# Performance work log

Measured on AMD Instinct MI355X. Metric: run time of the kernel, lower is better.

## Reference

```python
import jax, jax.numpy as jnp
import numpy as np

N_MICS = 8
REF_MIC = 0
DIAG_LOAD = 1e-5
PI_ITERS = 30  # power-iteration steps for principal eigenvector of Phi_nn^-1 Phi_ss


def setup_inputs() -> dict:
    key = jax.random.key(0)
    k1, k2, k3, k4 = jax.random.split(key, 4)
    B, M, F, T = 8, N_MICS, 257, 2000
    return {
        "spec_re": jax.random.normal(k1, (B, M, F, T), dtype=jnp.float32),
        "spec_im": jax.random.normal(k2, (B, M, F, T), dtype=jnp.float32),
        "speech_mask": jax.random.uniform(k3, (B, F, T), dtype=jnp.float32),
        "noise_mask": jax.random.uniform(k4, (B, F, T), dtype=jnp.float32),
    }


def _mvdr(spec_re, spec_im, speech_mask, noise_mask):
    # (B, M, F, T) complex STFT -> (B, F, M, T) for per-(batch, freq) processing
    Y = (spec_re + 1j * spec_im).astype(jnp.complex64)
    Y = jnp.transpose(Y, (0, 2, 1, 3))  # (B, F, M, T)
    M = Y.shape[2]

    def masked_cov(mask):  # mask: (B, F, T) real
        msum = mask.sum(-1) + 1e-8                       # (B, F)
        Yw = Y * mask[:, :, None, :]                      # (B, F, M, T)
        Phi = jnp.einsum('bfmt,bfnt->bfmn', Yw, Y.conj())  # (B, F, M, M)
        return Phi / msum[..., None, None]

    Phi_ss = masked_cov(speech_mask)
    eye = jnp.eye(M, dtype=jnp.complex64)
    Phi_nn = masked_cov(noise_mask) + DIAG_LOAD * eye

    Phi_nn_inv = jnp.linalg.inv(Phi_nn)                   # batched (B, F, M, M)
    G = jnp.einsum('bfmn,bfnk->bfmk', Phi_nn_inv, Phi_ss)

    # Principal eigenvector of G via power iteration (G has real, nonnegative
    # eigenvalues since it is similar to a Hermitian-PSD generalized pencil),
    # matching torch.linalg.eig + argmax(eigenvalues.real) up to scale.
    v = jnp.ones(G.shape[:-1], dtype=jnp.complex64)       # (B, F, M)
    for _ in range(PI_ITERS):
        v = jnp.einsum('bfmn,bfn->bfm', G, v)
        v = v / (jnp.linalg.norm(v, axis=-1, keepdims=True) + 1e-12)

    # Relative transfer function normalized to reference mic (removes scale)
    rtf = v / (v[..., REF_MIC:REF_MIC + 1] + 1e-8)        # (B, F, M)

    d = jnp.einsum('bfmn,bfn->bfm', Phi_nn_inv, rtf)      # Phi_nn^-1 rtf
    denom = jnp.einsum('bfm,bfm->bf', rtf.conj(), d).real + 1e-8
    w = d / denom[..., None]                              # (B, F, M) MVDR weights

    enhanced = jnp.einsum('bfm,bfmt->bft', w.conj(), Y)   # (B, F, T) complex
    return enhanced


def reference(spec_re, spec_im, speech_mask, noise_mask):
    return _mvdr(spec_re, spec_im, speech_mask, noise_mask)
```

## Files before the change

kernel.cpp:

```cpp
#include <hip/hip_runtime.h>

#define B_DIM 8
#define M_MICS 8
#define F_DIM 257
#define T_DIM 2000
#define NPROB (B_DIM * F_DIM)
#define TILE 256
#define NFULL 7
#define TAILW 208

__device__ float g_w[NPROB * 16];

#define GLOAD_LDS(g, s) __builtin_amdgcn_global_load_lds(                       \
    (const __attribute__((address_space(1))) void*)(g),                         \
    (__attribute__((address_space(3))) void*)(s), 16, 0, 0)


#define PAIR_ACC(a, bb, k)                                              \
    {                                                                   \
        const float pr = yr[a][u] * yr[bb][u] + yi[a][u] * yi[bb][u];   \
        const float pi = yi[a][u] * yr[bb][u] - yr[a][u] * yi[bb][u];   \
        acc[(k) + 0] += msv[u] * pr;                                    \
        acc[(k) + 1] += msv[u] * pi;                                    \
        acc[(k) + 2] += mnv[u] * pr;                                    \
        acc[(k) + 3] += mnv[u] * pi;                                    \
    }

#define LOADM(k, mic)                                                             \
    {                                                                             \
        const float4 vr_ = *reinterpret_cast<const float4*>(&lds[bb][mic][4 * l]);      \
        const float4 vi_ = *reinterpret_cast<const float4*>(&lds[bb][8 + (mic)][4 * l]);\
        yr[k][0] = vr_.x; yr[k][1] = vr_.y; yr[k][2] = vr_.z; yr[k][3] = vr_.w;   \
        yi[k][0] = vi_.x; yi[k][1] = vi_.y; yi[k][2] = vi_.z; yi[k][3] = vi_.w;   \
    }

#define PAIR_BODY(LOADS, ACCS, KM)                                      \
    {                                                                   \
        float yr[KM][4], yi[KM][4];                                     \
        LOADS                                                           \
        _Pragma("unroll")                                               \
        for (int u = 0; u < 4; ++u) { ACCS }                            \
    }

__launch_bounds__(512, 4)
__global__ void cov_solve_kernel(const float* __restrict__ sre, const float* __restrict__ sim,
                                 const float* __restrict__ smask, const float* __restrict__ nmask)
{
    const int f = blockIdx.x, b = blockIdx.y, tid = threadIdx.x;
    const int h = tid >> 6, l = tid & 63;

    __shared__ float lds[2][18][TILE];
    __shared__ float sG[8][20];

    const size_t mrow = (size_t)F_DIM * T_DIM;
    const size_t base_bf = ((size_t)(b * M_MICS) * F_DIM + f) * T_DIM;
    const size_t mbase   = ((size_t)b * F_DIM + f) * T_DIM;

    const float* g_re = sre + base_bf + (size_t)h * mrow;
    const float* g_im = sim + base_bf + (size_t)h * mrow;
    const float* g_ms = smask + mbase;
    const float* g_mn = nmask + mbase;

    float acc[18];
#pragma unroll
    for (int i = 0; i < 18; ++i) acc[i] = 0.f;

    auto STAGE = [&](int bb, int toff, int tw) {
        if (4 * l < tw) {
            GLOAD_LDS(g_re + toff + 4 * l, &lds[bb][h][0]);
            GLOAD_LDS(g_im + toff + 4 * l, &lds[bb][8 + h][0]);
            if (h == 0)      GLOAD_LDS(g_ms + toff + 4 * l, &lds[bb][16][0]);
            else if (h == 1) GLOAD_LDS(g_mn + toff + 4 * l, &lds[bb][17][0]);
        }
    };

    auto COMPUTE = [&](int bb) {
        float msv[4], mnv[4];
        {
            const float4 v = *reinterpret_cast<const float4*>(&lds[bb][16][4 * l]);
            msv[0] = v.x; msv[1] = v.y; msv[2] = v.z; msv[3] = v.w;
        }
        {
            const float4 v = *reinterpret_cast<const float4*>(&lds[bb][17][4 * l]);
            mnv[0] = v.x; mnv[1] = v.y; mnv[2] = v.z; mnv[3] = v.w;
        }
        if (h == 0) {
            acc[0] += msv[0] + msv[1] + msv[2] + msv[3];
            acc[1] += mnv[0] + mnv[1] + mnv[2] + mnv[3];
#pragma unroll
            for (int m = 0; m < 8; ++m) {
                const float4 re4 = *reinterpret_cast<const float4*>(&lds[bb][m][4 * l]);
                const float4 im4 = *reinterpret_cast<const float4*>(&lds[bb][8 + m][4 * l]);
                const float rr[4] = { re4.x, re4.y, re4.z, re4.w };
                const float ii[4] = { im4.x, im4.y, im4.z, im4.w };
#pragma unroll
                for (int u = 0; u < 4; ++u) {
                    const float pd = rr[u] * rr[u] + ii[u] * ii[u];
                    acc[2 + m]  += msv[u] * pd;
                    acc[10 + m] += mnv[u] * pd;
                }
            }
        } else if (h == 1) {
            PAIR_BODY(LOADM(0,0) LOADM(1,1) LOADM(2,2) LOADM(3,3) LOADM(4,4),
                      PAIR_ACC(0,1,0) PAIR_ACC(0,2,4) PAIR_ACC(0,3,8) PAIR_ACC(0,4,12), 5)
        } else if (h == 2) {
            PAIR_BODY(LOADM(0,0) LOADM(1,1) LOADM(2,2) LOADM(3,5) LOADM(4,6) LOADM(5,7),
                      PAIR_ACC(0,3,0) PAIR_ACC(0,4,4) PAIR_ACC(0,5,8) PAIR_ACC(1,2,12), 6)
        } else if (h == 3) {
            PAIR_BODY(LOADM(0,1) LOADM(1,3) LOADM(2,4) LOADM(3,5) LOADM(4,6),
                      PAIR_ACC(0,1,0) PAIR_ACC(0,2,4) PAIR_ACC(0,3,8) PAIR_ACC(0,4,12), 5)
        } else if (h == 4) {
            PAIR_BODY(LOADM(0,1) LOADM(1,2) LOADM(2,3) LOADM(3,4) LOADM(4,5) LOADM(5,7),
                      PAIR_ACC(0,5,0) PAIR_ACC(1,2,4) PAIR_ACC(1,3,8) PAIR_ACC(1,4,12), 6)
        } else if (h == 5) {
            PAIR_BODY(LOADM(0,2) LOADM(1,3) LOADM(2,4) LOADM(3,5) LOADM(4,6) LOADM(5,7),
                      PAIR_ACC(0,4,0) PAIR_ACC(0,5,4) PAIR_ACC(1,2,8) PAIR_ACC(1,3,12), 6)
        } else if (h == 6) {
            PAIR_BODY(LOADM(0,3) LOADM(1,4) LOADM(2,5) LOADM(3,6) LOADM(4,7),
                      PAIR_ACC(0,3,0) PAIR_ACC(0,4,4) PAIR_ACC(1,2,8) PAIR_ACC(1,3,12), 5)
        } else {
            PAIR_BODY(LOADM(0,4) LOADM(1,5) LOADM(2,6) LOADM(3,7),
                      PAIR_ACC(0,3,0) PAIR_ACC(1,2,4) PAIR_ACC(1,3,8) PAIR_ACC(2,3,12), 4)
        }
    };

    STAGE(0, 0, TILE);
    __syncthreads();
#pragma unroll 1
    for (int t = 0; t < NFULL; ++t) {
        if (t < NFULL - 1) STAGE((t + 1) & 1, (t + 1) * TILE, TILE);
        else               STAGE(1, NFULL * TILE, TAILW);
        const int bb = t & 1;
        COMPUTE(bb);
        __syncthreads();
    }
    if (4 * l < TAILW) {
        const int bb = 1;
        COMPUTE(bb);
    }

#pragma unroll
    for (int i = 0; i < 18; ++i) {
        acc[i] += __shfl_xor(acc[i], 1, 64);
        acc[i] += __shfl_xor(acc[i], 2, 64);
        acc[i] += __shfl_xor(acc[i], 4, 64);
        acc[i] += __shfl_xor(acc[i], 8, 64);
        acc[i] += __shfl_xor(acc[i], 16, 64);
        acc[i] += __shfl_xor(acc[i], 32, 64);
    }
    if (l == 0) {
#pragma unroll
        for (int i = 0; i < 18; ++i) sG[h][i] = acc[i];
    }
    __syncthreads();

    if (tid < 64) {
        const int r = tid >> 3, cc = tid & 7;
        const float Ssum = sG[0][0] + 1e-8f;
        const float Nsum = sG[0][1] + 1e-8f;

        float ssr, ssi, ar, ai;
        if (r == cc) {
            ssr = sG[0][2 + r] / Ssum;  ssi = 0.f;
            ar  = sG[0][10 + r] / Nsum + 1e-5f;  ai = 0.f;
        } else {
            const int mm  = (r < cc) ? r : cc;
            const int nn2 = (r < cc) ? cc : r;
            const int q = mm * 8 - mm * (mm + 1) / 2 + nn2 - mm - 1;
            const int g = 1 + (q >> 2);
            const int basei = 4 * (q & 3);
            const float sgn = (r < cc) ? 1.f : -1.f;
            ssr = sG[g][basei] / Ssum;
            ssi = sgn * sG[g][basei + 1] / Ssum;
            ar  = sG[g][basei + 2] / Nsum;
            ai  = sgn * sG[g][basei + 3] / Nsum;
        }

        float br = (r == cc) ? 1.f : 0.f, bi = 0.f;
        for (int k = 0; k < 8; ++k) {
            const float pr = __shfl(ar, k * 9, 64);
            const float pi = __shfl(ai, k * 9, 64);
            const float den = pr * pr + pi * pi;
            const float qr = pr / den, qi = -pi / den;
            const bool isk = (r == k);
            const float ar2 = ar * qr - ai * qi;
            const float ai2 = ar * qi + ai * qr;
            const float br2 = br * qr - bi * qi;
            const float bi2 = br * qi + bi * qr;
            ar = isk ? ar2 : ar; ai = isk ? ai2 : ai;
            br = isk ? br2 : br; bi = isk ? bi2 : bi;
            const float rar = __shfl(ar, k * 8 + cc, 64);
            const float rai = __shfl(ai, k * 8 + cc, 64);
            const float rbr = __shfl(br, k * 8 + cc, 64);
            const float rbi = __shfl(bi, k * 8 + cc, 64);
            const float fr = __shfl(ar, r * 8 + k, 64);
            const float fi = __shfl(ai, r * 8 + k, 64);
            const float uar = ar - (fr * rar - fi * rai);
            const float uai = ai - (fr * rai + fi * rar);
            const float ubr = br - (fr * rbr - fi * rbi);
            const float ubi = bi - (fr * rbi + fi * rbr);
            ar = isk ? ar : uar; ai = isk ? ai : uai;
            br = isk ? br : ubr; bi = isk ? bi : ubi;
        }

        float gr = 0.f, gi = 0.f;
        for (int k = 0; k < 8; ++k) {
            const float ir = __shfl(br, r * 8 + k, 64);
            const float ii = __shfl(bi, r * 8 + k, 64);
            const float skr = __shfl(ssr, k * 8 + cc, 64);
            const float ski = __shfl(ssi, k * 8 + cc, 64);
            gr += ir * skr - ii * ski;
            gi += ir * ski + ii * skr;
        }

        float vr = 1.f, vi = 0.f;
        for (int itp = 0; itp < 30; ++itp) {
            float wr2 = gr * vr - gi * vi;
            float wi2 = gr * vi + gi * vr;
            wr2 += __shfl_xor(wr2, 1, 64); wi2 += __shfl_xor(wi2, 1, 64);
            wr2 += __shfl_xor(wr2, 2, 64); wi2 += __shfl_xor(wi2, 2, 64);
            wr2 += __shfl_xor(wr2, 4, 64); wi2 += __shfl_xor(wi2, 4, 64);
            float nrm = wr2 * wr2 + wi2 * wi2;
            nrm += __shfl_xor(nrm, 8, 64);
            nrm += __shfl_xor(nrm, 16, 64);
            nrm += __shfl_xor(nrm, 32, 64);
            const float inv = 1.f / (sqrtf(nrm) + 1e-12f);
            wr2 *= inv; wi2 *= inv;
            vr = __shfl(wr2, cc * 9, 64);
            vi = __shfl(wi2, cc * 9, 64);
        }

        const float v0r = __shfl(vr, 0, 64) + 1e-8f;
        const float v0i = __shfl(vi, 0, 64);
        const float dd = v0r * v0r + v0i * v0i;
        const float rtr = (vr * v0r + vi * v0i) / dd;
        const float rti = (vi * v0r - vr * v0i) / dd;

        float dr = br * rtr - bi * rti;
        float di = br * rti + bi * rtr;
        dr += __shfl_xor(dr, 1, 64); di += __shfl_xor(di, 1, 64);
        dr += __shfl_xor(dr, 2, 64); di += __shfl_xor(di, 2, 64);
        dr += __shfl_xor(dr, 4, 64); di += __shfl_xor(di, 4, 64);

        float qden = (r == cc) ? (rtr * dr + rti * di) : 0.f;
        qden += __shfl_xor(qden, 1, 64); qden += __shfl_xor(qden, 2, 64);
        qden += __shfl_xor(qden, 4, 64); qden += __shfl_xor(qden, 8, 64);
        qden += __shfl_xor(qden, 16, 64); qden += __shfl_xor(qden, 32, 64);
        qden += 1e-8f;

        if (cc == 0) {
            const int p = b * F_DIM + f;
            g_w[p * 16 + r]     = dr / qden;
            g_w[p * 16 + 8 + r] = di / qden;
        }
    }
}

__launch_bounds__(256, 8)
__global__ void apply_kernel(const float* __restrict__ sre, const float* __restrict__ sim,
                             float* __restrict__ out, int out_mode)
{
    const int f = blockIdx.x, b = blockIdx.y, z = blockIdx.z;
    const int tid = threadIdx.x;
    __shared__ float sW[16];
    const int p = b * F_DIM + f;
    if (tid < 16) sW[tid] = g_w[p * 16 + tid];
    __syncthreads();

    const int t0 = z * 512 + 2 * tid;
    if (t0 >= T_DIM) return;

    const size_t mrow = (size_t)F_DIM * T_DIM;
    const size_t base_bf = ((size_t)(b * M_MICS) * F_DIM + f) * T_DIM;
    const size_t mbase   = ((size_t)b * F_DIM + f) * T_DIM;

    float er0 = 0.f, ei0 = 0.f, er1 = 0.f, ei1 = 0.f;
#pragma unroll
    for (int m = 0; m < 8; ++m) {
        const float2 vr2 = *reinterpret_cast<const float2*>(sre + base_bf + (size_t)m * mrow + t0);
        const float2 vi2 = *reinterpret_cast<const float2*>(sim + base_bf + (size_t)m * mrow + t0);
        const float wr = sW[m], wi = sW[8 + m];
        er0 += wr * vr2.x + wi * vi2.x;
        ei0 += wr * vi2.x - wi * vr2.x;
        er1 += wr * vr2.y + wi * vi2.y;
        ei1 += wr * vi2.y - wi * vr2.y;
    }
    if (out_mode == 2) {
        *reinterpret_cast<float4*>(out + 2 * (mbase + t0)) = make_float4(er0, ei0, er1, ei1);
    } else {
        *reinterpret_cast<float2*>(out + mbase + t0) = make_float2(er0, er1);
    }
}

extern "C" void kernel_launch(void* const* d_in, const int* in_sizes, int n_in,
                              void* d_out, int out_size, void* d_ws, size_t ws_size,
                              hipStream_t stream)
{
    const float* sre   = (const float*)d_in[0];
    const float* sim   = (const float*)d_in[1];
    const float* smask = (const float*)d_in[2];
    const float* nmask = (const float*)d_in[3];
    float* out = (float*)d_out;

    const int mode = (out_size >= 2 * B_DIM * F_DIM * T_DIM) ? 2 : 1;

    cov_solve_kernel<<<dim3(F_DIM, B_DIM), 512, 0, stream>>>(sre, sim, smask, nmask);
    apply_kernel<<<dim3(F_DIM, B_DIM, 4), 256, 0, stream>>>(sre, sim, out, mode);
}
```

Baseline: 178.4 us.

## Split covariance over time chunks, rebalance wave work, separate batched solve kernel

The covariance kernel now splits the 2000-frame time axis into two chunks via a third grid dimension. It writes partial covariance sums to a global scratch buffer. A new solve kernel adds the two partials and runs the inversion, power iteration and MVDR weight computation, packing four problems per block with one wavefront each. The pair assignment across the eight wavefronts is rebalanced so each does a similar number of mic-pair products. This is meant to raise parallelism, even out per-wave work and stop 448 threads sitting idle during the serial solve tail. The cost is an extra kernel launch and a global round-trip for the partial covariances.

```diff
diff --git a/kernel.cpp b/kernel.cpp
--- a/kernel.cpp
+++ b/kernel.cpp
@@ -6,9 +6,11 @@
 #define T_DIM 2000
 #define NPROB (B_DIM * F_DIM)
 #define TILE 256
-#define NFULL 7
-#define TAILW 208
-
+#define CHUNK 1000
+#define NTILE 4
+#define TAILW 232
+
+__device__ float g_cov[NPROB * 2 * 144];
 __device__ float g_w[NPROB * 16];
 
 #define GLOAD_LDS(g, s) __builtin_amdgcn_global_load_lds(                       \
@@ -16,54 +18,55 @@
     (__attribute__((address_space(3))) void*)(s), 16, 0, 0)
 
 
-#define PAIR_ACC(a, bb, k)                                              \
+#define PAIR_ACC(a, bb2, k)                                             \
     {                                                                   \
-        const float pr = yr[a][u] * yr[bb][u] + yi[a][u] * yi[bb][u];   \
-        const float pi = yi[a][u] * yr[bb][u] - yr[a][u] * yi[bb][u];   \
+        const float pr = yr[a][u] * yr[bb2][u] + yi[a][u] * yi[bb2][u]; \
+        const float pi = yi[a][u] * yr[bb2][u] - yr[a][u] * yi[bb2][u]; \
         acc[(k) + 0] += msv[u] * pr;                                    \
         acc[(k) + 1] += msv[u] * pi;                                    \
         acc[(k) + 2] += mnv[u] * pr;                                    \
         acc[(k) + 3] += mnv[u] * pi;                                    \
     }
 
-#define LOADM(k, mic)                                                             \
-    {                                                                             \
+#define LOADM(k, mic)                                                                   \
+    {                                                                                   \
         const float4 vr_ = *reinterpret_cast<const float4*>(&lds[bb][mic][4 * l]);      \
         const float4 vi_ = *reinterpret_cast<const float4*>(&lds[bb][8 + (mic)][4 * l]);\
-        yr[k][0] = vr_.x; yr[k][1] = vr_.y; yr[k][2] = vr_.z; yr[k][3] = vr_.w;   \
-        yi[k][0] = vi_.x; yi[k][1] = vi_.y; yi[k][2] = vi_.z; yi[k][3] = vi_.w;   \
-    }
-
-#define PAIR_BODY(LOADS, ACCS, KM)                                      \
-    {                                                                   \
-        float yr[KM][4], yi[KM][4];                                     \
-        LOADS                                                           \
-        _Pragma("unroll")                                               \
-        for (int u = 0; u < 4; ++u) { ACCS }                            \
+        yr[k][0] = vr_.x; yr[k][1] = vr_.y; yr[k][2] = vr_.z; yr[k][3] = vr_.w;         \
+        yi[k][0] = vi_.x; yi[k][1] = vi_.y; yi[k][2] = vi_.z; yi[k][3] = vi_.w;         \
+    }
+
+#define MASKS4                                                                   \
+    float msv[4], mnv[4];                                                        \
+    {                                                                            \
+        const float4 v = *reinterpret_cast<const float4*>(&lds[bb][16][4 * l]);  \
+        msv[0] = v.x; msv[1] = v.y; msv[2] = v.z; msv[3] = v.w;                  \
+        const float4 w = *reinterpret_cast<const float4*>(&lds[bb][17][4 * l]);  \
+        mnv[0] = w.x; mnv[1] = w.y; mnv[2] = w.z; mnv[3] = w.w;                  \
     }
 
 __launch_bounds__(512, 4)
-__global__ void cov_solve_kernel(const float* __restrict__ sre, const float* __restrict__ sim,
-                                 const float* __restrict__ smask, const float* __restrict__ nmask)
+__global__ void cov_kernel(const float* __restrict__ sre, const float* __restrict__ sim,
+                           const float* __restrict__ smask, const float* __restrict__ nmask)
 {
-    const int f = blockIdx.x, b = blockIdx.y, tid = threadIdx.x;
+    const int f = blockIdx.x, b = blockIdx.y, c = blockIdx.z;
+    const int tid = threadIdx.x;
     const int h = tid >> 6, l = tid & 63;
 
     __shared__ float lds[2][18][TILE];
-    __shared__ float sG[8][20];
 
     const size_t mrow = (size_t)F_DIM * T_DIM;
-    const size_t base_bf = ((size_t)(b * M_MICS) * F_DIM + f) * T_DIM;
-    const size_t mbase   = ((size_t)b * F_DIM + f) * T_DIM;
+    const size_t base_bf = ((size_t)(b * M_MICS) * F_DIM + f) * T_DIM + (size_t)c * CHUNK;
+    const size_t mbase   = ((size_t)b * F_DIM + f) * T_DIM + (size_t)c * CHUNK;
 
     const float* g_re = sre + base_bf + (size_t)h * mrow;
     const float* g_im = sim + base_bf + (size_t)h * mrow;
     const float* g_ms = smask + mbase;
     const float* g_mn = nmask + mbase;
 
-    float acc[18];
-#pragma unroll
-    for (int i = 0; i < 18; ++i) acc[i] = 0.f;
+    float acc[24];
+#pragma unroll
+    for (int i = 0; i < 24; ++i) acc[i] = 0.f;
 
     auto STAGE = [&](int bb, int toff, int tw) {
         if (4 * l < tw) {
@@ -74,73 +77,98 @@
         }
     };
 
-    auto COMPUTE = [&](int bb) {
-        float msv[4], mnv[4];
-        {
-            const float4 v = *reinterpret_cast<const float4*>(&lds[bb][16][4 * l]);
-            msv[0] = v.x; msv[1] = v.y; msv[2] = v.z; msv[3] = v.w;
-        }
-        {
-            const float4 v = *reinterpret_cast<const float4*>(&lds[bb][17][4 * l]);
-            mnv[0] = v.x; mnv[1] = v.y; mnv[2] = v.z; mnv[3] = v.w;
-        }
+    auto COMPUTE = [&](int bb, int tw) {
+        if (4 * l >= tw) return;
+        MASKS4
         if (h == 0) {
             acc[0] += msv[0] + msv[1] + msv[2] + msv[3];
             acc[1] += mnv[0] + mnv[1] + mnv[2] + mnv[3];
 #pragma unroll
-            for (int m = 0; m < 8; ++m) {
-                const float4 re4 = *reinterpret_cast<const float4*>(&lds[bb][m][4 * l]);
-                const float4 im4 = *reinterpret_cast<const float4*>(&lds[bb][8 + m][4 * l]);
+            for (int j = 0; j < 4; ++j) {
+                const float4 re4 = *reinterpret_cast<const float4*>(&lds[bb][j][4 * l]);
+                const float4 im4 = *reinterpret_cast<const float4*>(&lds[bb][8 + j][4 * l]);
                 const float rr[4] = { re4.x, re4.y, re4.z, re4.w };
                 const float ii[4] = { im4.x, im4.y, im4.z, im4.w };
 #pragma unroll
                 for (int u = 0; u < 4; ++u) {
                     const float pd = rr[u] * rr[u] + ii[u] * ii[u];
-                    acc[2 + m]  += msv[u] * pd;
-                    acc[10 + m] += mnv[u] * pd;
+                    acc[2 + j] += msv[u] * pd;
+                    acc[6 + j] += mnv[u] * pd;
                 }
             }
+        } else if (h == 7) {
+#pragma unroll
+            for (int j = 0; j < 4; ++j) {
+                const float4 re4 = *reinterpret_cast<const float4*>(&lds[bb][4 + j][4 * l]);
+                const float4 im4 = *reinterpret_cast<const float4*>(&lds[bb][12 + j][4 * l]);
+                const float rr[4] = { re4.x, re4.y, re4.z, re4.w };
+                const float ii[4] = { im4.x, im4.y, im4.z, im4.w };
+#pragma unroll
+                for (int u = 0; u < 4; ++u) {
+                    const float pd = rr[u] * rr[u] + ii[u] * ii[u];
+                    acc[j]     += msv[u] * pd;
+                    acc[4 + j] += mnv[u] * pd;
+                }
+            }
         } else if (h == 1) {
-            PAIR_BODY(LOADM(0,0) LOADM(1,1) LOADM(2,2) LOADM(3,3) LOADM(4,4),
-                      PAIR_ACC(0,1,0) PAIR_ACC(0,2,4) PAIR_ACC(0,3,8) PAIR_ACC(0,4,12), 5)
+            float yr[4][4], yi[4][4];
+            LOADM(0,0) LOADM(1,1) LOADM(2,2) LOADM(3,3)
+#pragma unroll
+            for (int u = 0; u < 4; ++u) {
+                PAIR_ACC(0,1,0) PAIR_ACC(0,2,4) PAIR_ACC(0,3,8)
+                PAIR_ACC(1,2,12) PAIR_ACC(1,3,16) PAIR_ACC(2,3,20)
+            }
         } else if (h == 2) {
-            PAIR_BODY(LOADM(0,0) LOADM(1,1) LOADM(2,2) LOADM(3,5) LOADM(4,6) LOADM(5,7),
-                      PAIR_ACC(0,3,0) PAIR_ACC(0,4,4) PAIR_ACC(0,5,8) PAIR_ACC(1,2,12), 6)
+            float yr[4][4], yi[4][4];
+            LOADM(0,4) LOADM(1,5) LOADM(2,6) LOADM(3,7)
+#pragma unroll
+            for (int u = 0; u < 4; ++u) {
+                PAIR_ACC(0,1,0) PAIR_ACC(0,2,4) PAIR_ACC(0,3,8)
+                PAIR_ACC(1,2,12) PAIR_ACC(1,3,16) PAIR_ACC(2,3,20)
+            }
         } else if (h == 3) {
-            PAIR_BODY(LOADM(0,1) LOADM(1,3) LOADM(2,4) LOADM(3,5) LOADM(4,6),
-                      PAIR_ACC(0,1,0) PAIR_ACC(0,2,4) PAIR_ACC(0,3,8) PAIR_ACC(0,4,12), 5)
+            float yr[4][4], yi[4][4];
+            LOADM(0,0) LOADM(1,1) LOADM(2,4) LOADM(3,5)
+#pragma unroll
+            for (int u = 0; u < 4; ++u) {
+                PAIR_ACC(0,2,0) PAIR_ACC(0,3,4) PAIR_ACC(1,2,8) PAIR_ACC(1,3,12)
+            }
         } else if (h == 4) {
-            PAIR_BODY(LOADM(0,1) LOADM(1,2) LOADM(2,3) LOADM(3,4) LOADM(4,5) LOADM(5,7),
-                      PAIR_ACC(0,5,0) PAIR_ACC(1,2,4) PAIR_ACC(1,3,8) PAIR_ACC(1,4,12), 6)
+            float yr[4][4], yi[4][4];
+            LOADM(0,0) LOADM(1,1) LOADM(2,6) LOADM(3,7)
+#pragma unroll
+            for (int u = 0; u < 4; ++u) {
+                PAIR_ACC(0,2,0) PAIR_ACC(0,3,4) PAIR_ACC(1,2,8) PAIR_ACC(1,3,12)
+            }
         } else if (h == 5) {
-            PAIR_BODY(LOADM(0,2) LOADM(1,3) LOADM(2,4) LOADM(3,5) LOADM(4,6) LOADM(5,7),
-                      PAIR_ACC(0,4,0) PAIR_ACC(0,5,4) PAIR_ACC(1,2,8) PAIR_ACC(1,3,12), 6)
-        } else if (h == 6) {
-            PAIR_BODY(LOADM(0,3) LOADM(1,4) LOADM(2,5) LOADM(3,6) LOADM(4,7),
-                      PAIR_ACC(0,3,0) PAIR_ACC(0,4,4) PAIR_ACC(1,2,8) PAIR_ACC(1,3,12), 5)
+            float yr[4][4], yi[4][4];
+            LOADM(0,2) LOADM(1,3) LOADM(2,4) LOADM(3,5)
+#pragma unroll
+            for (int u = 0; u < 4; ++u) {
+                PAIR_ACC(0,2,0) PAIR_ACC(0,3,4) PAIR_ACC(1,2,8) PAIR_ACC(1,3,12)
+            }
         } else {
-            PAIR_BODY(LOADM(0,4) LOADM(1,5) LOADM(2,6) LOADM(3,7),
-                      PAIR_ACC(0,3,0) PAIR_ACC(1,2,4) PAIR_ACC(1,3,8) PAIR_ACC(2,3,12), 4)
+            float yr[4][4], yi[4][4];
+            LOADM(0,2) LOADM(1,3) LOADM(2,6) LOADM(3,7)
+#pragma unroll
+            for (int u = 0; u < 4; ++u) {
+                PAIR_ACC(0,2,0) PAIR_ACC(0,3,4) PAIR_ACC(1,2,8) PAIR_ACC(1,3,12)
+            }
         }
     };
 
     STAGE(0, 0, TILE);
     __syncthreads();
 #pragma unroll 1
-    for (int t = 0; t < NFULL; ++t) {
-        if (t < NFULL - 1) STAGE((t + 1) & 1, (t + 1) * TILE, TILE);
-        else               STAGE(1, NFULL * TILE, TAILW);
-        const int bb = t & 1;
-        COMPUTE(bb);
+    for (int t = 0; t < NTILE; ++t) {
+        const int tw = (t == NTILE - 1) ? TAILW : TILE;
+        if (t < NTILE - 1) STAGE((t + 1) & 1, (t + 1) * TILE, (t + 1 == NTILE - 1) ? TAILW : TILE);
+        COMPUTE(t & 1, tw);
         __syncthreads();
     }
-    if (4 * l < TAILW) {
-        const int bb = 1;
-        COMPUTE(bb);
-    }
-
-#pragma unroll
-    for (int i = 0; i < 18; ++i) {
+
+#pragma unroll
+    for (int i = 0; i < 24; ++i) {
         acc[i] += __shfl_xor(acc[i], 1, 64);
         acc[i] += __shfl_xor(acc[i], 2, 64);
         acc[i] += __shfl_xor(acc[i], 4, 64);
@@ -148,111 +176,166 @@
         acc[i] += __shfl_xor(acc[i], 16, 64);
         acc[i] += __shfl_xor(acc[i], 32, 64);
     }
+
     if (l == 0) {
-#pragma unroll
-        for (int i = 0; i < 18; ++i) sG[h][i] = acc[i];
+        const int p = b * F_DIM + f;
+        float* dst = g_cov + ((size_t)p * 2 + c) * 144;
+        if (h == 0) {
+            dst[0] = acc[0]; dst[1] = acc[1];
+#pragma unroll
+            for (int j = 0; j < 4; ++j) { dst[2 + j] = acc[2 + j]; dst[10 + j] = acc[6 + j]; }
+        } else if (h == 7) {
+#pragma unroll
+            for (int j = 0; j < 4; ++j) { dst[6 + j] = acc[j]; dst[14 + j] = acc[4 + j]; }
+        } else if (h == 1) {
+            const int qs[6] = {0, 1, 2, 7, 8, 13};
+#pragma unroll
+            for (int i = 0; i < 6; ++i)
+#pragma unroll
+                for (int t2 = 0; t2 < 4; ++t2) dst[18 + 4 * qs[i] + t2] = acc[4 * i + t2];
+        } else if (h == 2) {
+            const int qs[6] = {22, 23, 24, 25, 26, 27};
+#pragma unroll
+            for (int i = 0; i < 6; ++i)
+#pragma unroll
+                for (int t2 = 0; t2 < 4; ++t2) dst[18 + 4 * qs[i] + t2] = acc[4 * i + t2];
+        } else if (h == 3) {
+            const int qs[4] = {3, 4, 9, 10};
+#pragma unroll
+            for (int i = 0; i < 4; ++i)
+#pragma unroll
+                for (int t2 = 0; t2 < 4; ++t2) dst[18 + 4 * qs[i] + t2] = acc[4 * i + t2];
+        } else if (h == 4) {
+            const int qs[4] = {5, 6, 11, 12};
+#pragma unroll
+            for (int i = 0; i < 4; ++i)
+#pragma unroll
+                for (int t2 = 0; t2 < 4; ++t2) dst[18 + 4 * qs[i] + t2] = acc[4 * i + t2];
+        } else if (h == 5) {
+            const int qs[4] = {14, 15, 18, 19};
+#pragma unroll
+            for (int i = 0; i < 4; ++i)
+#pragma unroll
+                for (int t2 = 0; t2 < 4; ++t2) dst[18 + 4 * qs[i] + t2] = acc[4 * i + t2];
+        } else {
+            const int qs[4] = {16, 17, 20, 21};
+#pragma unroll
+            for (int i = 0; i < 4; ++i)
+#pragma unroll
+                for (int t2 = 0; t2 < 4; ++t2) dst[18 + 4 * qs[i] + t2] = acc[4 * i + t2];
+        }
+    }
+}
+
+__launch_bounds__(256, 4)
+__global__ void solve_kernel()
+{
+    const int tid = threadIdx.x;
+    const int w = tid >> 6, lane = tid & 63;
+    const int p = blockIdx.x * 4 + w;
+
+    __shared__ float sPhi[4][144];
+    {
+        const float* s0 = g_cov + (size_t)p * 2 * 144;
+        for (int i = lane; i < 144; i += 64) sPhi[w][i] = s0[i] + s0[144 + i];
     }
     __syncthreads();
 
-    if (tid < 64) {
-        const int r = tid >> 3, cc = tid & 7;
-        const float Ssum = sG[0][0] + 1e-8f;
-        const float Nsum = sG[0][1] + 1e-8f;
-
-        float ssr, ssi, ar, ai;
-        if (r == cc) {
-            ssr = sG[0][2 + r] / Ssum;  ssi = 0.f;
-            ar  = sG[0][10 + r] / Nsum + 1e-5f;  ai = 0.f;
-        } else {
-            const int mm  = (r < cc) ? r : cc;
-            const int nn2 = (r < cc) ? cc : r;
-            const int q = mm * 8 - mm * (mm + 1) / 2 + nn2 - mm - 1;
-            const int g = 1 + (q >> 2);
-            const int basei = 4 * (q & 3);
-            const float sgn = (r < cc) ? 1.f : -1.f;
-            ssr = sG[g][basei] / Ssum;
-            ssi = sgn * sG[g][basei + 1] / Ssum;
-            ar  = sG[g][basei + 2] / Nsum;
-            ai  = sgn * sG[g][basei + 3] / Nsum;
-        }
-
-        float br = (r == cc) ? 1.f : 0.f, bi = 0.f;
-        for (int k = 0; k < 8; ++k) {
-            const float pr = __shfl(ar, k * 9, 64);
-            const float pi = __shfl(ai, k * 9, 64);
-            const float den = pr * pr + pi * pi;
-            const float qr = pr / den, qi = -pi / den;
-            const bool isk = (r == k);
-            const float ar2 = ar * qr - ai * qi;
-            const float ai2 = ar * qi + ai * qr;
-            const float br2 = br * qr - bi * qi;
-            const float bi2 = br * qi + bi * qr;
-            ar = isk ? ar2 : ar; ai = isk ? ai2 : ai;
-            br = isk ? br2 : br; bi = isk ? bi2 : bi;
-            const float rar = __shfl(ar, k * 8 + cc, 64);
-            const float rai = __shfl(ai, k * 8 + cc, 64);
-            const float rbr = __shfl(br, k * 8 + cc, 64);
-            const float rbi = __shfl(bi, k * 8 + cc, 64);
-            const float fr = __shfl(ar, r * 8 + k, 64);
-            const float fi = __shfl(ai, r * 8 + k, 64);
-            const float uar = ar - (fr * rar - fi * rai);
-            const float uai = ai - (fr * rai + fi * rar);
-            const float ubr = br - (fr * rbr - fi * rbi);
-            const float ubi = bi - (fr * rbi + fi * rbr);
-            ar = isk ? ar : uar; ai = isk ? ai : uai;
-            br = isk ? br : ubr; bi = isk ? bi : ubi;
-        }
-
-        float gr = 0.f, gi = 0.f;
-        for (int k = 0; k < 8; ++k) {
-            const float ir = __shfl(br, r * 8 + k, 64);
-            const float ii = __shfl(bi, r * 8 + k, 64);
-            const float skr = __shfl(ssr, k * 8 + cc, 64);
-            const float ski = __shfl(ssi, k * 8 + cc, 64);
-            gr += ir * skr - ii * ski;
-            gi += ir * ski + ii * skr;
-        }
-
-        float vr = 1.f, vi = 0.f;
-        for (int itp = 0; itp < 30; ++itp) {
-            float wr2 = gr * vr - gi * vi;
-            float wi2 = gr * vi + gi * vr;
-            wr2 += __shfl_xor(wr2, 1, 64); wi2 += __shfl_xor(wi2, 1, 64);
-            wr2 += __shfl_xor(wr2, 2, 64); wi2 += __shfl_xor(wi2, 2, 64);
-            wr2 += __shfl_xor(wr2, 4, 64); wi2 += __shfl_xor(wi2, 4, 64);
-            float nrm = wr2 * wr2 + wi2 * wi2;
-            nrm += __shfl_xor(nrm, 8, 64);
-            nrm += __shfl_xor(nrm, 16, 64);
-            nrm += __shfl_xor(nrm, 32, 64);
-            const float inv = 1.f / (sqrtf(nrm) + 1e-12f);
-            wr2 *= inv; wi2 *= inv;
-            vr = __shfl(wr2, cc * 9, 64);
-            vi = __shfl(wi2, cc * 9, 64);
-        }
-
-        const float v0r = __shfl(vr, 0, 64) + 1e-8f;
-        const float v0i = __shfl(vi, 0, 64);
-        const float dd = v0r * v0r + v0i * v0i;
-        const float rtr = (vr * v0r + vi * v0i) / dd;
-        const float rti = (vi * v0r - vr * v0i) / dd;
-
-        float dr = br * rtr - bi * rti;
-        float di = br * rti + bi * rtr;
-        dr += __shfl_xor(dr, 1, 64); di += __shfl_xor(di, 1, 64);
-        dr += __shfl_xor(dr, 2, 64); di += __shfl_xor(di, 2, 64);
-        dr += __shfl_xor(dr, 4, 64); di += __shfl_xor(di, 4, 64);
-
-        float qden = (r == cc) ? (rtr * dr + rti * di) : 0.f;
-        qden += __shfl_xor(qden, 1, 64); qden += __shfl_xor(qden, 2, 64);
-        qden += __shfl_xor(qden, 4, 64); qden += __shfl_xor(qden, 8, 64);
-        qden += __shfl_xor(qden, 16, 64); qden += __shfl_xor(qden, 32, 64);
-        qden += 1e-8f;
-
-        if (cc == 0) {
-            const int p = b * F_DIM + f;
-            g_w[p * 16 + r]     = dr / qden;
-            g_w[p * 16 + 8 + r] = di / qden;
-        }
+    const int r = lane >> 3, cc = lane & 7;
+    const float Ssum = sPhi[w][0] + 1e-8f;
+    const float Nsum = sPhi[w][1] + 1e-8f;
+
+    float ssr, ssi, ar, ai;
+    if (r == cc) {
+        ssr = sPhi[w][2 + r] / Ssum;  ssi = 0.f;
+        ar  = sPhi[w][10 + r] / Nsum + 1e-5f;  ai = 0.f;
+    } else {
+        const int mm  = (r < cc) ? r : cc;
+        const int nn2 = (r < cc) ? cc : r;
+        const int q = mm * 8 - mm * (mm + 1) / 2 + nn2 - mm - 1;
+        const int basei = 18 + 4 * q;
+        const float sgn = (r < cc) ? 1.f : -1.f;
+        ssr = sPhi[w][basei] / Ssum;
+        ssi = sgn * sPhi[w][basei + 1] / Ssum;
+        ar  = sPhi[w][basei + 2] / Nsum;
+        ai  = sgn * sPhi[w][basei + 3] / Nsum;
+    }
+
+    float br = (r == cc) ? 1.f : 0.f, bi = 0.f;
+    for (int k = 0; k < 8; ++k) {
+        const float pr = __shfl(ar, k * 9, 64);
+        const float pi = __shfl(ai, k * 9, 64);
+        const float den = pr * pr + pi * pi;
+        const float qr = pr / den, qi = -pi / den;
+        const bool isk = (r == k);
+        const float ar2 = ar * qr - ai * qi;
+        const float ai2 = ar * qi + ai * qr;
+        const float br2 = br * qr - bi * qi;
+        const float bi2 = br * qi + bi * qr;
+        ar = isk ? ar2 : ar; ai = isk ? ai2 : ai;
+        br = isk ? br2 : br; bi = isk ? bi2 : bi;
+        const float rar = __shfl(ar, k * 8 + cc, 64);
+        const float rai = __shfl(ai, k * 8 + cc, 64);
+        const float rbr = __shfl(br, k * 8 + cc, 64);
+        const float rbi = __shfl(bi, k * 8 + cc, 64);
+        const float fr = __shfl(ar, r * 8 + k, 64);
+        const float fi = __shfl(ai, r * 8 + k, 64);
+        const float uar = ar - (fr * rar - fi * rai);
+        const float uai = ai - (fr * rai + fi * rar);
+        const float ubr = br - (fr * rbr - fi * rbi);
+        const float ubi = bi - (fr * rbi + fi * rbr);
+        ar = isk ? ar : uar; ai = isk ? ai : uai;
+        br = isk ? br : ubr; bi = isk ? bi : ubi;
+    }
+
+    float gr = 0.f, gi = 0.f;
+    for (int k = 0; k < 8; ++k) {
+        const float ir = __shfl(br, r * 8 + k, 64);
+        const float ii = __shfl(bi, r * 8 + k, 64);
+        const float skr = __shfl(ssr, k * 8 + cc, 64);
+        const float ski = __shfl(ssi, k * 8 + cc, 64);
+        gr += ir * skr - ii * ski;
+        gi += ir * ski + ii * skr;
+    }
+
+    float vr = 1.f, vi = 0.f;
+    for (int itp = 0; itp < 30; ++itp) {
+        float wr2 = gr * vr - gi * vi;
+        float wi2 = gr * vi + gi * vr;
+        wr2 += __shfl_xor(wr2, 1, 64); wi2 += __shfl_xor(wi2, 1, 64);
+        wr2 += __shfl_xor(wr2, 2, 64); wi2 += __shfl_xor(wi2, 2, 64);
+        wr2 += __shfl_xor(wr2, 4, 64); wi2 += __shfl_xor(wi2, 4, 64);
+        float nrm = wr2 * wr2 + wi2 * wi2;
+        nrm += __shfl_xor(nrm, 8, 64);
+        nrm += __shfl_xor(nrm, 16, 64);
+        nrm += __shfl_xor(nrm, 32, 64);
+        const float inv = 1.f / (sqrtf(nrm) + 1e-12f);
+        wr2 *= inv; wi2 *= inv;
+        vr = __shfl(wr2, cc * 9, 64);
+        vi = __shfl(wi2, cc * 9, 64);
+    }
+
+    const float v0r = __shfl(vr, 0, 64) + 1e-8f;
+    const float v0i = __shfl(vi, 0, 64);
+    const float dd = v0r * v0r + v0i * v0i;
+    const float rtr = (vr * v0r + vi * v0i) / dd;
+    const float rti = (vi * v0r - vr * v0i) / dd;
+
+    float dr = br * rtr - bi * rti;
+    float di = br * rti + bi * rtr;
+    dr += __shfl_xor(dr, 1, 64); di += __shfl_xor(di, 1, 64);
+    dr += __shfl_xor(dr, 2, 64); di += __shfl_xor(di, 2, 64);
+    dr += __shfl_xor(dr, 4, 64); di += __shfl_xor(di, 4, 64);
+
+    float qden = (r == cc) ? (rtr * dr + rti * di) : 0.f;
+    qden += __shfl_xor(qden, 1, 64); qden += __shfl_xor(qden, 2, 64);
+    qden += __shfl_xor(qden, 4, 64); qden += __shfl_xor(qden, 8, 64);
+    qden += __shfl_xor(qden, 16, 64); qden += __shfl_xor(qden, 32, 64);
+    qden += 1e-8f;
+
+    if (cc == 0) {
+        g_w[p * 16 + r]     = dr / qden;
+        g_w[p * 16 + 8 + r] = di / qden;
     }
 }
 
@@ -304,6 +387,7 @@
 
     const int mode = (out_size >= 2 * B_DIM * F_DIM * T_DIM) ? 2 : 1;
 
-    cov_solve_kernel<<<dim3(F_DIM, B_DIM), 512, 0, stream>>>(sre, sim, smask, nmask);
+    cov_kernel<<<dim3(F_DIM, B_DIM, 2), 512, 0, stream>>>(sre, sim, smask, nmask);
+    solve_kernel<<<dim3(NPROB / 4), 256, 0, stream>>>();
     apply_kernel<<<dim3(F_DIM, B_DIM, 4), 256, 0, stream>>>(sre, sim, out, mode);
 }
```

Result: faster. 161.3 us (-9.6%).
